# Kernel tuning notes

Measured on AMD Instinct MI355X. Metric: run time of the kernel, lower is better.

The kernel has to match this reference:

```python
import jax, jax.numpy as jnp
import numpy as np

# Loihi neuron constants (from a typical slayerSNN network.yaml)
I_DECAY = 1024.0   # current decay (of 4096)
V_DECAY = 128.0    # voltage decay (of 4096)
THETA = 100.0      # firing threshold


def spike_loihi(x):
    """Loihi CUBA neuron dynamics over trailing time axis. x: [..., T] weighted input."""
    xT = jnp.moveaxis(x, -1, 0)  # [T, ...]
    a_i = (4096.0 - I_DECAY) / 4096.0
    a_v = (4096.0 - V_DECAY) / 4096.0

    def step(carry, xt):
        u, v = carry
        u = a_i * u + xt           # synaptic current
        v = a_v * v + u            # membrane voltage
        s = (v >= THETA).astype(x.dtype)
        v = v * (1.0 - s)          # reset on spike
        return (u, v), s

    z = jnp.zeros(xT.shape[1:], x.dtype)
    _, s = jax.lax.scan(step, (z, z), xT)
    return jnp.moveaxis(s, 0, -1)


def delay_shift(x):
    """Shift spikes by 1 timestep along last axis (slayer.delayShift(spike, 1))."""
    return jnp.concatenate([jnp.zeros_like(x[..., :1]), x[..., :-1]], axis=-1)


def conv_t(x, w):
    """Per-timestep 2D conv, padding 1. x: [N,C,H,W,T], w: [O,I,3,3]."""
    N, C, H, W, T = x.shape
    xt = jnp.transpose(x, (0, 4, 1, 2, 3)).reshape(N * T, C, H, W)
    y = jax.lax.conv_general_dilated(xt, w, (1, 1), [(1, 1), (1, 1)],
                                     dimension_numbers=('NCHW', 'OIHW', 'NCHW'))
    O = w.shape[0]
    return jnp.transpose(y.reshape(N, T, O, H, W), (0, 2, 3, 4, 1))


def sum_pool2(x, w):
    """slayer.pool(2): 2x2 sum-pool scaled by (loaded) scalar pool weight."""
    N, C, H, W, T = x.shape
    return x.reshape(N, C, H // 2, 2, W // 2, 2, T).sum(axis=(3, 5)) * w


def setup_inputs() -> dict:
    key = jax.random.key(0)
    ks = jax.random.split(key, 8)
    N, T = 16, 128
    spike = jax.random.bernoulli(ks[0], 0.1, (N, 2, 40, 40, T)).astype(jnp.float32)
    conv1_w = jax.random.normal(ks[1], (8, 2, 3, 3), jnp.float32) * 0.5
    conv2_w = jax.random.normal(ks[2], (16, 8, 3, 3), jnp.float32) * 0.05
    conv3_w = jax.random.normal(ks[3], (32, 16, 3, 3), jnp.float32) * 0.05
    fc1_w = jax.random.normal(ks[4], (512, 10 * 10 * 32), jnp.float32) * 0.02
    pool1_w = jnp.asarray(1.1, jnp.float32)
    pool2_w = jnp.asarray(1.1, jnp.float32)
    return {"spike": spike, "conv1_w": conv1_w, "conv2_w": conv2_w,
            "conv3_w": conv3_w, "pool1_w": pool1_w, "pool2_w": pool2_w,
            "fc1_w": fc1_w}


def reference(spike, conv1_w, conv2_w, conv3_w, pool1_w, pool2_w, fc1_w):
    x = spike_loihi(conv_t(spike, conv1_w * 20.0))    # weightScale=20
    x = delay_shift(x)
    x = spike_loihi(sum_pool2(x, pool1_w))
    x = delay_shift(x)
    x = spike_loihi(conv_t(x, conv2_w * 100.0))       # weightScale=100
    x = delay_shift(x)
    x = spike_loihi(sum_pool2(x, pool2_w))
    x = delay_shift(x)
    x = spike_loihi(conv_t(x, conv3_w * 100.0))       # weightScale=100
    N, T = x.shape[0], x.shape[-1]
    x = x.reshape(N, -1, 1, 1, T)                     # [N, 3200, 1, 1, T]
    x = delay_shift(x)
    x = spike_loihi(jnp.einsum('nchwt,oc->nohwt', x, fc1_w))
    x = delay_shift(x)
    return x
```

## Files before the change

kernel.cpp:

```cpp
#include <hip/hip_runtime.h>
#include <stdint.h>


#define T 128
#define AI 0.75f
#define AV 0.96875f
#define THETA 100.0f

typedef __attribute__((ext_vector_type(8))) short v8s;
typedef __attribute__((ext_vector_type(16))) float v16f;

__device__ __forceinline__ void neuron_step(float x, float& u, float& v, float& s) {
    u = AI * u + x;
    v = AV * v + u;
    s = (v >= THETA) ? 1.0f : 0.0f;
    v = v * (1.0f - s);
}

__global__ __launch_bounds__(256) void conv1_prep(
    const float* __restrict__ in, const float* __restrict__ cw,
    uint8_t* __restrict__ sout,
    const float* __restrict__ fw, const float* __restrict__ c2w,
    const float* __restrict__ c3w, uint16_t* __restrict__ bs,
    uint16_t* __restrict__ apk, uint16_t* __restrict__ s2P,
    uint16_t* __restrict__ s4P)
{
    __shared__ float ldsF[64 * 130];
    int tid = threadIdx.x;

    if (blockIdx.x >= 3200) {
        int pbid = blockIdx.x - 3200;
        if (pbid < 1600) {
            int i = pbid * 256 + tid;
            float4 wv = *(const float4*)(fw + i * 4);
            float w4[4] = {wv.x, wv.y, wv.z, wv.w};
            uint16_t h[4], m[4], l[4];
            #pragma unroll
            for (int j = 0; j < 4; j++) {
                uint32_t b0 = __float_as_uint(w4[j]);
                h[j] = (uint16_t)(b0 >> 16);
                float r1 = w4[j] - __uint_as_float(b0 & 0xFFFF0000u);
                uint32_t b1 = __float_as_uint(r1);
                m[j] = (uint16_t)(b1 >> 16);
                float r2 = r1 - __uint_as_float(b1 & 0xFFFF0000u);
                l[j] = (uint16_t)(__float_as_uint(r2) >> 16);
            }
            *(ushort4*)(bs +       0 + i * 4) = make_ushort4(h[0], h[1], h[2], h[3]);
            *(ushort4*)(bs + 1638400 + i * 4) = make_ushort4(m[0], m[1], m[2], m[3]);
            *(ushort4*)(bs + 3276800 + i * 4) = make_ushort4(l[0], l[1], l[2], l[3]);
        } else if (pbid < 1614) {
            int unit = (pbid - 1600) * 4 + (tid >> 6);
            if (unit >= 54) return;
            int conv = unit / 27;
            int plane = (unit % 27) / 9;
            int dlt = unit % 9;
            int lane = tid & 63;
            int o = lane & 31, chi = (lane >> 5) * 8;
            int CO = conv ? 32 : 16;
            int CI = conv ? 16 : 8;
            const float* Wp = conv ? c3w : c2w;
            uint32_t wb[4] = {0u, 0u, 0u, 0u};
            #pragma unroll
            for (int e = 0; e < 8; e++) {
                int c = chi + e;
                float w = (o < CO && c < CI) ? Wp[((size_t)o * CI + c) * 9 + dlt] : 0.f;
                uint32_t b0 = __float_as_uint(w);
                uint16_t hi = (uint16_t)(b0 >> 16);
                float r1 = w - __uint_as_float(b0 & 0xFFFF0000u);
                uint32_t b1 = __float_as_uint(r1);
                uint16_t md = (uint16_t)(b1 >> 16);
                float r2 = r1 - __uint_as_float(b1 & 0xFFFF0000u);
                uint16_t lo = (uint16_t)(__float_as_uint(r2) >> 16);
                uint32_t pv = (plane == 0) ? hi : ((plane == 1) ? md : lo);
                wb[e >> 1] |= pv << ((e & 1) * 16);
            }
            *(uint4*)(apk + ((size_t)conv * 27 + plane * 9 + dlt) * 512 + lane * 8) =
                make_uint4(wb[0], wb[1], wb[2], wb[3]);
        } else {
            int hid = pbid - 1614;
            uint8_t* dst;
            if (hid < 1344) {
                int n = hid / 84, r = hid % 84;
                int hy, wx;
                if (r < 22)      { hy = 0;  wx = r; }
                else if (r < 44) { hy = 21; wx = r - 22; }
                else { int r2 = r - 44; hy = 1 + (r2 >> 1); wx = (r2 & 1) ? 21 : 0; }
                dst = (uint8_t*)s2P + ((size_t)(n * 484) + hy * 22 + wx) * 4096;
            } else {
                int h2 = hid - 1344;
                int n = h2 / 44, r = h2 % 44;
                int hy, wx;
                if (r < 12)      { hy = 0;  wx = r; }
                else if (r < 24) { hy = 11; wx = r - 12; }
                else { int r2 = r - 24; hy = 1 + (r2 >> 1); wx = (r2 & 1) ? 11 : 0; }
                dst = (uint8_t*)s4P + ((size_t)(n * 144) + hy * 12 + wx) * 4096;
            }
            *(uint4*)(dst + tid * 16) = make_uint4(0u, 0u, 0u, 0u);
        }
        return;
    }

    int bid0 = blockIdx.x;
    int bid = (bid0 & 7) * 400 + (bid0 >> 3);
    int wg = bid % 5;
    int hy = (bid / 5) % 40;
    int n  = bid / 200;
    int wxl = tid >> 5, tt = tid & 31, t0 = tt * 4;
    int wx = wg * 8 + wxl;

    float4 tap[18];
    #pragma unroll
    for (int c = 0; c < 2; c++)
      #pragma unroll
      for (int dh = 0; dh < 3; dh++)
        #pragma unroll
        for (int dw = 0; dw < 3; dw++) {
            int q = c * 9 + dh * 3 + dw;
            int hh = hy + dh - 1, ww = wx + dw - 1;
            bool ok = (hh >= 0) && (hh < 40) && (ww >= 0) && (ww < 40);
            tap[q] = ok ? *(const float4*)(in +
                (((size_t)(n * 2 + c) * 40 + hh) * 40 + ww) * T + t0)
                        : make_float4(0.f, 0.f, 0.f, 0.f);
        }

    #pragma unroll
    for (int o = 0; o < 8; o++) {
        const float* wp = cw + o * 18;
        float a0 = 0.f, a1 = 0.f, a2 = 0.f, a3 = 0.f;
        #pragma unroll
        for (int q = 0; q < 18; q++) {
            a0 += wp[q] * tap[q].x;  a1 += wp[q] * tap[q].y;
            a2 += wp[q] * tap[q].z;  a3 += wp[q] * tap[q].w;
        }
        float* xr = &ldsF[(o * 8 + wxl) * 130 + t0];
        xr[0] = a0 * 20.0f; xr[1] = a1 * 20.0f;
        xr[2] = a2 * 20.0f; xr[3] = a3 * 20.0f;
    }
    __syncthreads();
    if (tid < 64) {
        int o = tid >> 3, wxl2 = tid & 7;
        float u = 0.f, v = 0.f;
        uint32_t ob[32];
        const float* xr = &ldsF[tid * 130];
        #pragma unroll
        for (int tb = 0; tb < 32; tb++) {
            float s0, s1, s2, s3;
            neuron_step(xr[tb * 4 + 0], u, v, s0);
            neuron_step(xr[tb * 4 + 1], u, v, s1);
            neuron_step(xr[tb * 4 + 2], u, v, s2);
            neuron_step(xr[tb * 4 + 3], u, v, s3);
            ob[tb] = (uint32_t)s0 | ((uint32_t)s1 << 8) |
                     ((uint32_t)s2 << 16) | ((uint32_t)s3 << 24);
        }
        uint32_t* op = (uint32_t*)(sout +
            (((size_t)(n * 8 + o) * 40 + hy) * 40 + wg * 8 + wxl2) * T);
        #pragma unroll
        for (int k = 0; k < 8; k++)
            *(uint4*)&op[k * 4] =
                make_uint4(ob[k*4], ob[k*4+1], ob[k*4+2], ob[k*4+3]);
    }
}

template<int C, int CB, int HO, int WO>
__global__ __launch_bounds__(64) void pool_pad(
    const uint8_t* __restrict__ in, const float* __restrict__ pw_ptr,
    uint16_t* __restrict__ sP)
{
    constexpr int ROWS = C * CB;
    constexpr int GP = (HO * WO) / CB;
    __shared__ uint8_t raw[ROWS * 132];
    uint32_t* ldsF = (uint32_t*)raw;
    uint8_t*  sbuf = raw;

    int bid = blockIdx.x;
    int grp = bid % GP, n = bid / GP;
    int tid = threadIdx.x;
    float pw = pw_ptr[0];

    float u = 0.f, v = 0.f;
    uint32_t ob[32];
    uint32_t carry = 0;

    #pragma unroll
    for (int tb = 0; tb < 2; tb++) {
        __syncthreads();
        #pragma unroll
        for (int k = 0; k < 4; k++) {
            int f = tid + k * 64;
            int row = f >> 2, q = f & 3;
            int c = row / CB, p = row % CB;
            int hw = grp * CB + p;
            int wx = hw % WO, hy = hw / WO;
            const uint8_t* p00 = in +
                (((size_t)(n * C + c) * (2 * HO) + 2 * hy) * (2 * WO) + 2 * wx) * T;
            int off = tb * 64 + q * 16;
            uint4 a = *(const uint4*)(p00 + off);
            uint4 b = *(const uint4*)(p00 + T + off);
            uint4 cc = *(const uint4*)(p00 + 2 * WO * T + off);
            uint4 d = *(const uint4*)(p00 + 2 * WO * T + T + off);
            *(uint4*)&ldsF[row * 20 + q * 4] =
                make_uint4(a.x + b.x + cc.x + d.x, a.y + b.y + cc.y + d.y,
                           a.z + b.z + cc.z + d.z, a.w + b.w + cc.w + d.w);
        }
        __syncthreads();
        #pragma unroll
        for (int q = 0; q < 4; q++) {
            uint4 w = *(const uint4*)&ldsF[tid * 20 + q * 4];
            uint32_t words[4] = {w.x, w.y, w.z, w.w};
            #pragma unroll
            for (int j = 0; j < 4; j++) {
                uint32_t cur = words[j];
                uint32_t del = (cur << 8) | carry;
                carry = cur >> 24;
                float s0, s1, s2, s3;
                neuron_step(pw * (float)(del & 0xffu),         u, v, s0);
                neuron_step(pw * (float)((del >> 8) & 0xffu),  u, v, s1);
                neuron_step(pw * (float)((del >> 16) & 0xffu), u, v, s2);
                neuron_step(pw * (float)((del >> 24) & 0xffu), u, v, s3);
                ob[tb * 16 + q * 4 + j] = (uint32_t)s0 | ((uint32_t)s1 << 8) |
                                          ((uint32_t)s2 << 16) | ((uint32_t)s3 << 24);
            }
        }
    }

    __syncthreads();
    #pragma unroll
    for (int j = 0; j < 32; j++)
        *(uint32_t*)&sbuf[tid * 132 + j * 4] = ob[j];
    __syncthreads();

    constexpr int CHK = CB * 128;
    #pragma unroll
    for (int k = 0; k < CHK / 64; k++) {
        int ci = k * 64 + tid;
        int p = ci >> 7, tau = ci & 127;
        int hw = grp * CB + p;
        int wx = hw % WO, hy = hw / WO;
        uint32_t wb[8];
        #pragma unroll
        for (int e = 0; e < 16; e += 2) {
            uint32_t lo = 0u, hi = 0u;
            if (tau >= 1) {
                if (e < C)     lo = sbuf[(e * CB + p) * 132 + tau - 1] ? 0x3F80u : 0u;
                if (e + 1 < C) hi = sbuf[((e + 1) * CB + p) * 132 + tau - 1] ? 0x3F80u : 0u;
            }
            wb[e >> 1] = lo | (hi << 16);
        }
        uint16_t* dst = sP + ((size_t)((n * (HO + 2) + hy + 1) * (WO + 2)
                                       + wx + 1)) * 2048 + tau * 16;
        *(uint4*)dst       = make_uint4(wb[0], wb[1], wb[2], wb[3]);
        *(uint4*)(dst + 8) = make_uint4(wb[4], wb[5], wb[6], wb[7]);
    }
}

template<int COUT, int PB, int H, int W>
__global__ __launch_bounds__(256, 2) void conv_scan_mfma(
    const uint16_t* __restrict__ sP, const uint16_t* __restrict__ apk,
    float scale, uint8_t* __restrict__ sout)
{
    constexpr int ROWS = COUT * PB;
    __shared__ float ldsF[ROWS * 130];
    constexpr int HW = H * W;
    constexpr int GP = HW / PB;
    int per = (16 * GP) >> 3;
    int vbid = (blockIdx.x & 7) * per + (blockIdx.x >> 3);
    int n = vbid / GP, grp = vbid % GP;
    int tid = threadIdx.x;
    int wv = tid >> 6, lane = tid & 63;
    int l31 = lane & 31, lhi = lane >> 5;
    int t0 = wv * 32;

    const uint16_t* ap = apk + (size_t)lane * 8;
    v8s a0[9], a1[9], a2[9];
    #pragma unroll
    for (int d = 0; d < 9; d++) {
        a0[d] = *(const v8s*)(ap + d * 512);
        a1[d] = *(const v8s*)(ap + (9 + d) * 512);
        a2[d] = *(const v8s*)(ap + (18 + d) * 512);
    }

    #pragma unroll
    for (int p = 0; p < PB; p++) {
        int hw = grp * PB + p;
        int hy = hw / W, wx = hw % W;
        v8s bfr[9];
        #pragma unroll
        for (int d = 0; d < 9; d++) {
            int dh = d / 3, dw = d % 3;
            const uint16_t* src = sP
                + ((size_t)((n * (H + 2) + hy + dh) * (W + 2) + wx + dw)) * 2048
                + (t0 + l31) * 16 + lhi * 8;
            bfr[d] = *(const v8s*)src;
        }
        v16f ac0, ac1, ac2;
        #pragma unroll
        for (int e = 0; e < 16; e++) { ac0[e] = 0.f; ac1[e] = 0.f; ac2[e] = 0.f; }
        #pragma unroll
        for (int d = 0; d < 9; d++) {
            ac0 = __builtin_amdgcn_mfma_f32_32x32x16_bf16(a0[d], bfr[d], ac0, 0, 0, 0);
            ac1 = __builtin_amdgcn_mfma_f32_32x32x16_bf16(a1[d], bfr[d], ac1, 0, 0, 0);
            ac2 = __builtin_amdgcn_mfma_f32_32x32x16_bf16(a2[d], bfr[d], ac2, 0, 0, 0);
        }
        constexpr int NR = (COUT == 32) ? 16 : 8;
        #pragma unroll
        for (int r = 0; r < NR; r++) {
            int o = (r & 3) + 8 * (r >> 2) + 4 * lhi;
            ldsF[(o * PB + p) * 130 + t0 + l31] =
                (ac0[r] + ac1[r] + ac2[r]) * scale;
        }
    }
    __syncthreads();
    if (tid < ROWS) {
        int o = tid / PB, p = tid % PB;
        int hw = grp * PB + p;
        float u = 0.f, v = 0.f;
        uint32_t ob[32];
        const float* xr = &ldsF[tid * 130];
        #pragma unroll
        for (int tb = 0; tb < 32; tb++) {
            float2 xa = *(const float2*)(xr + tb * 4);
            float2 xb = *(const float2*)(xr + tb * 4 + 2);
            float s0, s1, s2, s3;
            neuron_step(xa.x, u, v, s0); neuron_step(xa.y, u, v, s1);
            neuron_step(xb.x, u, v, s2); neuron_step(xb.y, u, v, s3);
            ob[tb] = (uint32_t)s0 | ((uint32_t)s1 << 8) |
                     ((uint32_t)s2 << 16) | ((uint32_t)s3 << 24);
        }
        uint32_t* op = (uint32_t*)(sout + ((size_t)(n * COUT + o) * HW + hw) * 128);
        #pragma unroll
        for (int k = 0; k < 8; k++)
            *(uint4*)&op[k * 4] =
                make_uint4(ob[k*4], ob[k*4+1], ob[k*4+2], ob[k*4+3]);
    }
}

__global__ __launch_bounds__(256) void sT_bf16(
    const uint8_t* __restrict__ s5, uint16_t* __restrict__ At)
{
    __shared__ uint8_t tile[64 * 132];
    int bid = blockIdx.x;
    int n = bid / 50;
    int c0 = (bid % 50) * 64;
    int tid = threadIdx.x;
    {
        int row = tid >> 2, q = tid & 3;
        const uint8_t* src = s5 + ((size_t)(n * 3200 + c0 + row)) * T + q * 32;
        *(uint4*)&tile[row * 132 + q * 32]      = *(const uint4*)src;
        *(uint4*)&tile[row * 132 + q * 32 + 16] = *(const uint4*)(src + 16);
    }
    __syncthreads();
    int t = tid >> 1, half = tid & 1;
    uint32_t wb[16];
    if (t == 0) {
        #pragma unroll
        for (int j = 0; j < 16; j++) wb[j] = 0u;
    } else {
        #pragma unroll
        for (int j = 0; j < 16; j++) {
            uint32_t lo = tile[(half * 32 + 2 * j) * 132 + (t - 1)] ? 0x3F80u : 0u;
            uint32_t hi = tile[(half * 32 + 2 * j + 1) * 132 + (t - 1)] ? 0x3F80u : 0u;
            wb[j] = lo | (hi << 16);
        }
    }
    uint16_t* dst = At + ((size_t)(n * 128 + t)) * 3200 + c0 + half * 32;
    #pragma unroll
    for (int k = 0; k < 4; k++)
        *(uint4*)(dst + k * 8) = make_uint4(wb[k*4], wb[k*4+1], wb[k*4+2], wb[k*4+3]);
}

#define GLDS16(g, s) __builtin_amdgcn_global_load_lds( \
    (const __attribute__((address_space(1))) uint32_t*)(g), \
    (__attribute__((address_space(3))) uint32_t*)(s), 16, 0, 0)

__global__ __launch_bounds__(512, 4) void fc_gemm_mfma(
    const uint16_t* __restrict__ At,
    const uint16_t* __restrict__ Bs,
    float* __restrict__ ypart)
{
    __shared__ uint8_t lds[65536];
    int bid0 = blockIdx.x;
    int bid = (bid0 & 7) * 80 + (bid0 >> 3);
    int n  = bid & 15;
    int ob = (bid >> 4) & 3;
    int ks = bid >> 6;
    int o0 = ob * 128;
    int cbase = ks * 320;

    int tid = threadIdx.x;
    int w8 = tid >> 6;
    int wm = w8 >> 2;
    int wn = w8 & 3;
    int lane = tid & 63;
    int l31 = lane & 31;
    int lhi = lane >> 5;
    int rb = lane >> 3;
    int gsw = (lane & 7) ^ (rb & 7);

    v16f acc[2];
    #pragma unroll
    for (int mi = 0; mi < 2; mi++)
        #pragma unroll
        for (int e = 0; e < 16; e++) acc[mi][e] = 0.0f;

    const uint16_t* Abase = At + (size_t)(n * 128) * 3200 + gsw * 8;

    for (int kc = 0; kc < 5; kc++) {
        int c0 = cbase + kc * 64;
        #pragma unroll
        for (int i = 0; i < 2; i++) {
            int cid = i * 8 + w8;
            const uint16_t* src = Abase + (size_t)(cid * 8 + rb) * 3200 + c0;
            GLDS16(src, lds + cid * 1024);
        }
        #pragma unroll
        for (int j = 0; j < 6; j++) {
            int cid = j * 8 + w8;
            int f0 = cid * 1024;
            int s = f0 >> 14;
            int r = ((f0 & 16383) >> 7) + rb;
            const uint16_t* src = Bs + (size_t)(s * 512 + o0 + r) * 3200
                                     + c0 + gsw * 8;
            GLDS16(src, lds + 16384 + f0);
        }
        __syncthreads();
        #pragma unroll
        for (int kf = 0; kf < 4; kf++) {
            int gc = kf * 2 + lhi;
            v8s av[2];
            #pragma unroll
            for (int mi = 0; mi < 2; mi++) {
                int t = wm * 64 + mi * 32 + l31;
                av[mi] = *(const v8s*)(lds + t * 128 + ((gc ^ (t & 7)) << 4));
            }
            #pragma unroll
            for (int s = 0; s < 3; s++) {
                int r = wn * 32 + l31;
                v8s bv = *(const v8s*)(lds + 16384 + s * 16384 + r * 128
                                       + ((gc ^ (r & 7)) << 4));
                #pragma unroll
                for (int mi = 0; mi < 2; mi++)
                    acc[mi] = __builtin_amdgcn_mfma_f32_32x32x16_bf16(
                        av[mi], bv, acc[mi], 0, 0, 0);
            }
        }
        __syncthreads();
    }
    float* yp = ypart + (size_t)ks * 1048576 + (size_t)n * 65536;
    int o = o0 + wn * 32 + l31;
    #pragma unroll
    for (int mi = 0; mi < 2; mi++) {
        #pragma unroll
        for (int r = 0; r < 16; r++) {
            int trow = wm * 64 + mi * 32 + (r & 3) + 8 * (r >> 2) + 4 * lhi;
            yp[trow * 512 + o] = acc[mi][r];
        }
    }
}

__global__ __launch_bounds__(256) void fc_scan(
    const float* __restrict__ yp,
    float* __restrict__ out)
{
    __shared__ float ldsX[16 * 132];
    int b = blockIdx.x;
    int n = b >> 5;
    int o0 = (b & 31) * 16;
    int tid = threadIdx.x;
    int t16 = tid >> 4, ol = tid & 15;
    const float* base = yp + (size_t)n * 65536 + o0 + ol;

    #pragma unroll
    for (int tb = 0; tb < 8; tb++) {
        int t = tb * 16 + t16;
        float x = base[(size_t)t * 512];
        #pragma unroll
        for (int k = 1; k < 10; k++)
            x += base[(size_t)k * 1048576 + (size_t)t * 512];
        ldsX[ol * 132 + t] = x;
    }
    __syncthreads();
    if (tid < 16) {
        int o = o0 + tid;
        const float* xr = &ldsX[tid * 132];
        float u = 0.f, v = 0.f;
        float prev = 0.f;
        float* op = out + ((size_t)(n * 512 + o)) * T;
        for (int tb = 0; tb < 32; tb++) {
            float bv[4];
            #pragma unroll
            for (int j = 0; j < 4; j++) {
                float s;
                neuron_step(xr[tb * 4 + j], u, v, s);
                bv[j] = prev; prev = s;
            }
            *(float4*)&op[tb * 4] = make_float4(bv[0], bv[1], bv[2], bv[3]);
        }
    }
}

extern "C" void kernel_launch(void* const* d_in, const int* in_sizes, int n_in,
                              void* d_out, int out_size, void* d_ws, size_t ws_size,
                              hipStream_t stream) {
    const float* spike = (const float*)d_in[0];
    const float* c1w   = (const float*)d_in[1];
    const float* c2w   = (const float*)d_in[2];
    const float* c3w   = (const float*)d_in[3];
    const float* p1w   = (const float*)d_in[4];
    const float* p2w   = (const float*)d_in[5];
    const float* fcw   = (const float*)d_in[6];
    float* out = (float*)d_out;

    char* ws = (char*)d_ws;
    uint8_t*  s1    = (uint8_t*)(ws);
    uint16_t* Bs16  = (uint16_t*)(ws + 26214400);
    uint16_t* Apk   = (uint16_t*)(ws + 36044800);
    uint16_t* s2P   = (uint16_t*)(ws + 36100096);
    uint8_t*  s3    = (uint8_t*)(ws + 67819520);
    uint16_t* s4P   = (uint16_t*)(ws + 80926720);
    uint8_t*  s5    = (uint8_t*)(ws + 90363904);
    uint16_t* At16  = (uint16_t*)(ws + 96917504);
    float*    ypart = (float*)(ws + 110024704);

    conv1_prep<<<6862, 256, 0, stream>>>(spike, c1w, s1,
                                         fcw, c2w, c3w, Bs16, Apk, s2P, s4P);

    pool_pad<8, 8, 20, 20><<<800, 64, 0, stream>>>(s1, p1w, s2P);
    conv_scan_mfma<16, 4, 20, 20><<<1600, 256, 0, stream>>>(s2P, Apk, 100.0f, s3);

    pool_pad<16, 4, 10, 10><<<400, 64, 0, stream>>>(s3, p2w, s4P);
    conv_scan_mfma<32, 2, 10, 10><<<800, 256, 0, stream>>>(s4P, Apk + 13824, 100.0f, s5);

    sT_bf16<<<800, 256, 0, stream>>>(s5, At16);
    fc_gemm_mfma<<<640, 512, 0, stream>>>(At16, Bs16, ypart);
    fc_scan<<<512, 256, 0, stream>>>(ypart, out);
}
```

Baseline: 231.2 us.

## Fuse conv3 scan with spike transpose into bf16 GEMM operand, permute FC weights

Merges the conv3 MFMA+neuron-scan kernel with the transpose-to-bf16 kernel so each block writes its spikes straight into the FC GEMM A matrix, skipping the uint8 s5 round trip and one launch. Because the fused block emits channels grouped by pixel pair rather than channel-major, the FC weight split in the prep kernel now gathers weights with a permuted index. The cost is scalar gathered loads of fc weights in place of float4 loads, plus extra LDS and two barriers in the fused kernel.

```diff
diff --git a/kernel.cpp b/kernel.cpp
--- a/kernel.cpp
+++ b/kernel.cpp
@@ -31,23 +31,26 @@
     if (blockIdx.x >= 3200) {
         int pbid = blockIdx.x - 3200;
         if (pbid < 1600) {
-            int i = pbid * 256 + tid;
-            float4 wv = *(const float4*)(fw + i * 4);
-            float w4[4] = {wv.x, wv.y, wv.z, wv.w};
+            int i4 = (pbid * 256 + tid) * 4;
             uint16_t h[4], m[4], l[4];
             #pragma unroll
             for (int j = 0; j < 4; j++) {
-                uint32_t b0 = __float_as_uint(w4[j]);
+                int flat = i4 + j;
+                int o = flat / 3200;
+                int cp = flat - o * 3200;
+                int orig = o * 3200 + (cp & 31) * 100 + (cp >> 5);
+                float w = fw[orig];
+                uint32_t b0 = __float_as_uint(w);
                 h[j] = (uint16_t)(b0 >> 16);
-                float r1 = w4[j] - __uint_as_float(b0 & 0xFFFF0000u);
+                float r1 = w - __uint_as_float(b0 & 0xFFFF0000u);
                 uint32_t b1 = __float_as_uint(r1);
                 m[j] = (uint16_t)(b1 >> 16);
                 float r2 = r1 - __uint_as_float(b1 & 0xFFFF0000u);
                 l[j] = (uint16_t)(__float_as_uint(r2) >> 16);
             }
-            *(ushort4*)(bs +       0 + i * 4) = make_ushort4(h[0], h[1], h[2], h[3]);
-            *(ushort4*)(bs + 1638400 + i * 4) = make_ushort4(m[0], m[1], m[2], m[3]);
-            *(ushort4*)(bs + 3276800 + i * 4) = make_ushort4(l[0], l[1], l[2], l[3]);
+            *(ushort4*)(bs +       0 + i4) = make_ushort4(h[0], h[1], h[2], h[3]);
+            *(ushort4*)(bs + 1638400 + i4) = make_ushort4(m[0], m[1], m[2], m[3]);
+            *(ushort4*)(bs + 3276800 + i4) = make_ushort4(l[0], l[1], l[2], l[3]);
         } else if (pbid < 1614) {
             int unit = (pbid - 1600) * 4 + (tid >> 6);
             if (unit >= 54) return;
@@ -334,38 +337,101 @@
     }
 }
 
-__global__ __launch_bounds__(256) void sT_bf16(
-    const uint8_t* __restrict__ s5, uint16_t* __restrict__ At)
+__global__ __launch_bounds__(256, 2) void conv3_scan_at(
+    const uint16_t* __restrict__ sP, const uint16_t* __restrict__ apk,
+    float scale, uint16_t* __restrict__ At)
 {
-    __shared__ uint8_t tile[64 * 132];
-    int bid = blockIdx.x;
-    int n = bid / 50;
-    int c0 = (bid % 50) * 64;
+    __shared__ float ldsF[64 * 130];
+    __shared__ uint8_t sbuf[64 * 132];
+    constexpr int W = 10, HW = 100, PB = 2, GP = 50;
+    int per = (16 * GP) >> 3;
+    int vbid = (blockIdx.x & 7) * per + (blockIdx.x >> 3);
+    int n = vbid / GP, grp = vbid % GP;
     int tid = threadIdx.x;
+    int wv = tid >> 6, lane = tid & 63;
+    int l31 = lane & 31, lhi = lane >> 5;
+    int t0 = wv * 32;
+
+    const uint16_t* ap = apk + (size_t)lane * 8;
+    v8s a0[9], a1[9], a2[9];
+    #pragma unroll
+    for (int d = 0; d < 9; d++) {
+        a0[d] = *(const v8s*)(ap + d * 512);
+        a1[d] = *(const v8s*)(ap + (9 + d) * 512);
+        a2[d] = *(const v8s*)(ap + (18 + d) * 512);
+    }
+
+    #pragma unroll
+    for (int p = 0; p < PB; p++) {
+        int hw = grp * PB + p;
+        int hy = hw / W, wx = hw % W;
+        v8s bfr[9];
+        #pragma unroll
+        for (int d = 0; d < 9; d++) {
+            int dh = d / 3, dw = d % 3;
+            const uint16_t* src = sP
+                + ((size_t)((n * 12 + hy + dh) * 12 + wx + dw)) * 2048
+                + (t0 + l31) * 16 + lhi * 8;
+            bfr[d] = *(const v8s*)src;
+        }
+        v16f ac0, ac1, ac2;
+        #pragma unroll
+        for (int e = 0; e < 16; e++) { ac0[e] = 0.f; ac1[e] = 0.f; ac2[e] = 0.f; }
+        #pragma unroll
+        for (int d = 0; d < 9; d++) {
+            ac0 = __builtin_amdgcn_mfma_f32_32x32x16_bf16(a0[d], bfr[d], ac0, 0, 0, 0);
+            ac1 = __builtin_amdgcn_mfma_f32_32x32x16_bf16(a1[d], bfr[d], ac1, 0, 0, 0);
+            ac2 = __builtin_amdgcn_mfma_f32_32x32x16_bf16(a2[d], bfr[d], ac2, 0, 0, 0);
+        }
+        #pragma unroll
+        for (int r = 0; r < 16; r++) {
+            int o = (r & 3) + 8 * (r >> 2) + 4 * lhi;
+            ldsF[(o * PB + p) * 130 + t0 + l31] =
+                (ac0[r] + ac1[r] + ac2[r]) * scale;
+        }
+    }
+    __syncthreads();
+    if (tid < 64) {
+        int o = tid / PB, p = tid % PB;
+        float u = 0.f, v = 0.f;
+        uint32_t ob[32];
+        const float* xr = &ldsF[tid * 130];
+        #pragma unroll
+        for (int tb = 0; tb < 32; tb++) {
+            float2 xa = *(const float2*)(xr + tb * 4);
+            float2 xb = *(const float2*)(xr + tb * 4 + 2);
+            float s0, s1, s2, s3;
+            neuron_step(xa.x, u, v, s0); neuron_step(xa.y, u, v, s1);
+            neuron_step(xb.x, u, v, s2); neuron_step(xb.y, u, v, s3);
+            ob[tb] = (uint32_t)s0 | ((uint32_t)s1 << 8) |
+                     ((uint32_t)s2 << 16) | ((uint32_t)s3 << 24);
+        }
+        int row = p * 32 + o;
+        #pragma unroll
+        for (int j = 0; j < 32; j++)
+            *(uint32_t*)&sbuf[row * 132 + j * 4] = ob[j];
+    }
+    __syncthreads();
     {
-        int row = tid >> 2, q = tid & 3;
-        const uint8_t* src = s5 + ((size_t)(n * 3200 + c0 + row)) * T + q * 32;
-        *(uint4*)&tile[row * 132 + q * 32]      = *(const uint4*)src;
-        *(uint4*)&tile[row * 132 + q * 32 + 16] = *(const uint4*)(src + 16);
-    }
-    __syncthreads();
-    int t = tid >> 1, half = tid & 1;
-    uint32_t wb[16];
-    if (t == 0) {
-        #pragma unroll
-        for (int j = 0; j < 16; j++) wb[j] = 0u;
-    } else {
-        #pragma unroll
-        for (int j = 0; j < 16; j++) {
-            uint32_t lo = tile[(half * 32 + 2 * j) * 132 + (t - 1)] ? 0x3F80u : 0u;
-            uint32_t hi = tile[(half * 32 + 2 * j + 1) * 132 + (t - 1)] ? 0x3F80u : 0u;
-            wb[j] = lo | (hi << 16);
-        }
-    }
-    uint16_t* dst = At + ((size_t)(n * 128 + t)) * 3200 + c0 + half * 32;
-    #pragma unroll
-    for (int k = 0; k < 4; k++)
-        *(uint4*)(dst + k * 8) = make_uint4(wb[k*4], wb[k*4+1], wb[k*4+2], wb[k*4+3]);
+        int t = tid >> 1, half = tid & 1;
+        uint32_t wb[16];
+        if (t == 0) {
+            #pragma unroll
+            for (int j = 0; j < 16; j++) wb[j] = 0u;
+        } else {
+            #pragma unroll
+            for (int j = 0; j < 16; j++) {
+                uint32_t lo = sbuf[(half * 32 + 2 * j) * 132 + (t - 1)] ? 0x3F80u : 0u;
+                uint32_t hi = sbuf[(half * 32 + 2 * j + 1) * 132 + (t - 1)] ? 0x3F80u : 0u;
+                wb[j] = lo | (hi << 16);
+            }
+        }
+        uint16_t* dst = At + ((size_t)(n * 128 + t)) * 3200 + grp * 64 + half * 32;
+        #pragma unroll
+        for (int k = 0; k < 4; k++)
+            *(uint4*)(dst + k * 8) =
+                make_uint4(wb[k*4], wb[k*4+1], wb[k*4+2], wb[k*4+3]);
+    }
 }
 
 #define GLDS16(g, s) __builtin_amdgcn_global_load_lds( \
@@ -517,7 +583,6 @@
     uint16_t* s2P   = (uint16_t*)(ws + 36100096);
     uint8_t*  s3    = (uint8_t*)(ws + 67819520);
     uint16_t* s4P   = (uint16_t*)(ws + 80926720);
-    uint8_t*  s5    = (uint8_t*)(ws + 90363904);
     uint16_t* At16  = (uint16_t*)(ws + 96917504);
     float*    ypart = (float*)(ws + 110024704);
 
@@ -528,9 +593,8 @@
     conv_scan_mfma<16, 4, 20, 20><<<1600, 256, 0, stream>>>(s2P, Apk, 100.0f, s3);
 
     pool_pad<16, 4, 10, 10><<<400, 64, 0, stream>>>(s3, p2w, s4P);
-    conv_scan_mfma<32, 2, 10, 10><<<800, 256, 0, stream>>>(s4P, Apk + 13824, 100.0f, s5);
-
-    sT_bf16<<<800, 256, 0, stream>>>(s5, At16);
+    conv3_scan_at<<<800, 256, 0, stream>>>(s4P, Apk + 13824, 100.0f, At16);
+
     fc_gemm_mfma<<<640, 512, 0, stream>>>(At16, Bs16, ypart);
     fc_scan<<<512, 256, 0, stream>>>(ypart, out);
 }
```

Measured after the change: 230.0 us. Within noise of the previous version (-0.5%).
